# Performance work log

Measured on AMD Instinct MI355X. Metric: run time of the kernel, lower is better.

## Reference

```python
import jax, jax.numpy as jnp
import numpy as np


def _gumbel(key, shape):
    # -log(Exp(1)) == standard Gumbel; matches torch's -empty.exponential_().log()
    u = jax.random.uniform(key, shape, minval=1e-10, maxval=1.0)
    return -jnp.log(-jnp.log(u))


def setup_inputs() -> dict:
    key = jax.random.key(0)
    dims = [(1026, 1024), (3074, 1024), (5122, 512)]
    names = ['wc1', 'wc2', 'wd1', 'wd2', 'gc1', 'gc2', 'gd1', 'gd2']
    inp = {}
    k = key
    for li, (din, dout) in enumerate(dims, start=1):
        for nm in names:
            k, sub = jax.random.split(k)
            if nm.startswith('w'):
                inp[f'l{li}_{nm}'] = jax.random.normal(sub, (din, dout), dtype=jnp.float32)
            else:
                inp[f'l{li}_{nm}'] = _gumbel(sub, (din, dout)).astype(jnp.float32)
    k, kx, kw = jax.random.split(k, 3)
    inp['x'] = jax.random.uniform(kx, (32768, 512), dtype=jnp.float32)
    inp['lin_w'] = jax.random.uniform(kw, (1, 1024), dtype=jnp.float32)
    inp['tau'] = 1
    return inp


def _st_gate(w, g, tau):
    # hard gumbel-softmax over axis 0 with straight-through estimator
    y = jax.nn.softmax((w + g) / tau, axis=0)
    hard = jax.nn.one_hot(jnp.argmax(y, axis=0), w.shape[0], dtype=y.dtype).T
    return hard + y - jax.lax.stop_gradient(y)


def _logic_layer(h, ws, gs, tau, skip):
    wc1, wc2, wd1, wd2 = ws
    gc1, gc2, gd1, gd2 = gs
    c = (h @ _st_gate(wc1, gc1, tau)) * (h @ _st_gate(wc2, gc2, tau))  # AND
    a = h @ _st_gate(wd1, gd1, tau)
    b = h @ _st_gate(wd2, gd2, tau)
    d = 1.0 - (1.0 - a) * (1.0 - b)  # OR
    parts = [h, c, d] if skip else [c, d]
    return jnp.concatenate(parts, axis=-1)


def reference(x, l1_wc1, l1_wc2, l1_wd1, l1_wd2, l1_gc1, l1_gc2, l1_gd1, l1_gd2,
              l2_wc1, l2_wc2, l2_wd1, l2_wd2, l2_gc1, l2_gc2, l2_gd1, l2_gd2,
              l3_wc1, l3_wc2, l3_wd1, l3_wd2, l3_gc1, l3_gc2, l3_gd1, l3_gd2,
              lin_w, tau):
    t = jnp.asarray(tau, dtype=x.dtype)
    B = x.shape[0]
    # InputAugmentor: [x, 1-x, 1, 0]
    h = jnp.concatenate([x, 1.0 - x, jnp.ones((B, 1), x.dtype), jnp.zeros((B, 1), x.dtype)], axis=-1)
    layers = [
        ((l1_wc1, l1_wc2, l1_wd1, l1_wd2), (l1_gc1, l1_gc2, l1_gd1, l1_gd2), True),
        ((l2_wc1, l2_wc2, l2_wd1, l2_wd2), (l2_gc1, l2_gc2, l2_gd1, l2_gd2), True),
        ((l3_wc1, l3_wc2, l3_wd1, l3_wd2), (l3_gc1, l3_gc2, l3_gd1, l3_gd2), False),
    ]
    for ws, gs, skip in layers:
        h = _logic_layer(h, ws, gs, t, skip)
    # nonnegative == False -> weight used as-is
    return (h @ lin_w.T).squeeze(-1)
```

## Files before the change

kernel.cpp:

```cpp
#include <hip/hip_runtime.h>
#include <hip/hip_fp16.h>
#include <stdint.h>


struct GatePtrs {
    const float* w[12];
    const float* g[12];
};

__device__ __forceinline__ unsigned int sortkey(float f) {
    unsigned int u = __float_as_uint(f);
    return u ^ ((u & 0x80000000u) ? 0xFFFFFFFFu : 0x80000000u);
}

__global__ __launch_bounds__(256) void argmax_part(GatePtrs gp,
                                                   unsigned long long* __restrict__ part) {
    const int dins[3]  = {1026, 3074, 5122};
    const int douts[3] = {1024, 1024, 512};
    const int chs[3]   = {65, 193, 321};
    const int pbs[3]   = {0, 266240, 1056768};
    int gate = blockIdx.z, layer = gate >> 2, slot = gate & 3;
    int din = dins[layer], dout = douts[layer], ch = chs[layer];
    int s4    = dout >> 2;
    int cols4 = s4;
    int sub   = threadIdx.x / cols4;
    int c4    = threadIdx.x - sub * cols4;
    int chunk = blockIdx.y * (256 / cols4) + sub;
    if (chunk >= ch) return;
    int r0 = chunk * 16;
    int n  = min(16, din - r0);
    const float4* __restrict__ wp = (const float4*)gp.w[gate] + (size_t)r0 * s4 + c4;
    const float4* __restrict__ gq = (const float4*)gp.g[gate] + (size_t)r0 * s4 + c4;
    float bx = -3.4e38f, by = bx, bz = bx, bw = bx;
    int ix = r0, iy = r0, iz = r0, iw = r0;
    if (n == 16) {
        #pragma unroll
        for (int u = 0; u < 4; ++u) {
            float4 wv[4], gv[4];
            #pragma unroll
            for (int k = 0; k < 4; ++k) {
                wv[k] = wp[(size_t)(u * 4 + k) * s4];
                gv[k] = gq[(size_t)(u * 4 + k) * s4];
            }
            #pragma unroll
            for (int k = 0; k < 4; ++k) {
                int i = r0 + u * 4 + k;
                float vx = wv[k].x + gv[k].x, vy = wv[k].y + gv[k].y;
                float vz = wv[k].z + gv[k].z, vw = wv[k].w + gv[k].w;
                if (vx > bx) { bx = vx; ix = i; }
                if (vy > by) { by = vy; iy = i; }
                if (vz > bz) { bz = vz; iz = i; }
                if (vw > bw) { bw = vw; iw = i; }
            }
        }
    } else {
        for (int m = 0; m < n; ++m) {
            float4 wv = wp[(size_t)m * s4];
            float4 gv = gq[(size_t)m * s4];
            int i = r0 + m;
            float vx = wv.x + gv.x, vy = wv.y + gv.y;
            float vz = wv.z + gv.z, vw = wv.w + gv.w;
            if (vx > bx) { bx = vx; ix = i; }
            if (vy > by) { by = vy; iy = i; }
            if (vz > bz) { bz = vz; iz = i; }
            if (vw > bw) { bw = vw; iw = i; }
        }
    }
    unsigned long long* dst = part + pbs[layer]
                            + ((size_t)(slot * ch + chunk)) * dout + 4 * c4;
    dst[0] = ((unsigned long long)sortkey(bx) << 32) | (unsigned int)ix;
    dst[1] = ((unsigned long long)sortkey(by) << 32) | (unsigned int)iy;
    dst[2] = ((unsigned long long)sortkey(bz) << 32) | (unsigned int)iz;
    dst[3] = ((unsigned long long)sortkey(bw) << 32) | (unsigned int)iw;
}

__global__ __launch_bounds__(256) void reduce_pairs2(const unsigned long long* __restrict__ part,
                                                     unsigned short* __restrict__ pf) {
    __shared__ unsigned long long red[256];
    int t = threadIdx.x;
    int k = t >> 5, gi = t & 31;
    int C = blockIdx.x * 32;
    int l, s, g0, half, dout, ch, pb;
    if (C < 4096)      { l = 0; s = C >> 10;          g0 = C & 1023;          half = 1024; dout = 1024; ch = 65;  pb = 0; }
    else if (C < 8192) { l = 1; s = (C - 4096) >> 10; g0 = (C - 4096) & 1023; half = 1024; dout = 1024; ch = 193; pb = 266240; }
    else               { l = 2; s = (C - 8192) >> 9;  g0 = (C - 8192) & 511;  half = 512;  dout = 512;  ch = 321; pb = 1056768; }
    int g = g0 + gi;
    const unsigned long long* __restrict__ p = part + pb + (size_t)(s * ch) * dout + g;
    unsigned long long best = 0;
    for (int c = k; c < ch; c += 8) {
        unsigned long long v = p[(size_t)c * dout];
        if ((unsigned int)(v >> 32) > (unsigned int)(best >> 32)) best = v;
    }
    red[t] = best;
    __syncthreads();
    #pragma unroll
    for (int st = 4; st >= 1; st >>= 1) {
        if (k < st) {
            unsigned long long o = red[t + st * 32];
            if ((unsigned int)(o >> 32) > (unsigned int)(best >> 32)) best = o;
            red[t] = best;
        }
        __syncthreads();
    }
    if (k == 0) {
        int type = s >> 1, e = s & 1;
        int j = 2 * (l * 2048 + type * half + g) + e;
        pf[j] = (unsigned short)best;
    }
}

__global__ __launch_bounds__(256) void argmax_atomic(GatePtrs gp,
                                                     unsigned long long* __restrict__ packed) {
    const int dins[3]  = {1026, 3074, 5122};
    const int douts[3] = {1024, 1024, 512};
    const int offs[3]  = {0, 4096, 8192};
    int gate = blockIdx.z, layer = gate >> 2;
    int din = dins[layer], dout = douts[layer];
    int c2 = blockIdx.x * 256 + threadIdx.x;
    int r0 = blockIdx.y * 64;
    if (2 * c2 >= dout || r0 >= din) return;
    int r1 = min(r0 + 64, din);
    const float* __restrict__ w = gp.w[gate];
    const float* __restrict__ g = gp.g[gate];
    float bx = -3.4e38f, by = -3.4e38f;
    int rx = r0, ry = r0;
    #pragma unroll 8
    for (int i = r0; i < r1; ++i) {
        float2 wv = *(const float2*)(w + (size_t)i * dout + 2 * c2);
        float2 gv = *(const float2*)(g + (size_t)i * dout + 2 * c2);
        float vx = wv.x + gv.x, vy = wv.y + gv.y;
        if (vx > bx) { bx = vx; rx = i; }
        if (vy > by) { by = vy; ry = i; }
    }
    unsigned long long* dst = packed + offs[layer] + (gate & 3) * dout + 2 * c2;
    atomicMax(dst, ((unsigned long long)sortkey(bx) << 32)
                   | (unsigned long long)(0xFFFFFFFFu - (unsigned int)rx));
    atomicMax(dst + 1, ((unsigned long long)sortkey(by) << 32)
                   | (unsigned long long)(0xFFFFFFFFu - (unsigned int)ry));
}

__global__ __launch_bounds__(256) void convert_fb(const unsigned long long* __restrict__ packed,
                                                  ushort2* __restrict__ pf) {
    int i = blockIdx.x * 256 + threadIdx.x;
    if (i >= 5120) return;
    int l    = (i < 2048) ? 0 : ((i < 4096) ? 1 : 2);
    int half = (l == 2) ? 512 : 1024;
    int r    = i - l * 2048;
    int type = (r >= half) ? 1 : 0;
    int g    = r - type * half;
    int o1   = l * 4096 + 2 * type * half + g;
    int o2   = o1 + half;
    unsigned int i1 = 0xFFFFFFFFu - (unsigned int)(packed[o1] & 0xFFFFFFFFull);
    unsigned int i2 = 0xFFFFFFFFu - (unsigned int)(packed[o2] & 0xFFFFFFFFull);
    pf[i] = make_ushort2((unsigned short)i1, (unsigned short)i2);
}

__device__ __forceinline__ __half2 bc(unsigned int u) { return __builtin_bit_cast(__half2, u); }
__device__ __forceinline__ unsigned int cb(__half2 h) { return __builtin_bit_cast(unsigned int, h); }

__device__ __forceinline__ uint2 gat(const char* hb, unsigned int s) {
    return *(const uint2*)(hb + (s << 3));
}
__device__ __forceinline__ uint2 andg(uint2 a, uint2 b) {
    return make_uint2(cb(__hmul2(bc(a.x), bc(b.x))), cb(__hmul2(bc(a.y), bc(b.y))));
}
__device__ __forceinline__ uint2 org(uint2 a, uint2 b) {
    __half2 one = __float2half2_rn(1.0f);
    __half2 lo = __hsub2(one, __hmul2(__hsub2(one, bc(a.x)), __hsub2(one, bc(b.x))));
    __half2 hi = __hsub2(one, __hmul2(__hsub2(one, bc(a.y)), __hsub2(one, bc(b.y))));
    return make_uint2(cb(lo), cb(hi));
}

__global__ __launch_bounds__(512) void forward_kernel(const float* __restrict__ x,
                                                      const float* __restrict__ lin_w,
                                                      const ushort2* __restrict__ pairs,
                                                      float* __restrict__ out) {
    __shared__ uint2 h[5122];
    __shared__ float4 red[8];
    const int t  = threadIdx.x;
    const int r0 = blockIdx.x * 4;
    const char* hb = (const char*)h;

    float xa = x[(size_t)(r0 + 0) * 512 + t];
    float xb = x[(size_t)(r0 + 1) * 512 + t];
    float xc = x[(size_t)(r0 + 2) * 512 + t];
    float xd = x[(size_t)(r0 + 3) * 512 + t];
    ushort2 pa0 = pairs[t], pa1 = pairs[512 + t];
    ushort2 po0 = pairs[1024 + t], po1 = pairs[1536 + t];
    h[t]       = make_uint2(cb(__floats2half2_rn(xa, xb)), cb(__floats2half2_rn(xc, xd)));
    h[512 + t] = make_uint2(cb(__floats2half2_rn(1.f - xa, 1.f - xb)),
                            cb(__floats2half2_rn(1.f - xc, 1.f - xd)));
    if (t == 0) {
        unsigned int o = cb(__float2half2_rn(1.0f));
        h[1024] = make_uint2(o, o);
        h[1025] = make_uint2(0u, 0u);
    }
    __syncthreads();

    {
        uint2 a0 = andg(gat(hb, pa0.x), gat(hb, pa0.y));
        uint2 a1 = andg(gat(hb, pa1.x), gat(hb, pa1.y));
        uint2 o0 = org(gat(hb, po0.x), gat(hb, po0.y));
        uint2 o1 = org(gat(hb, po1.x), gat(hb, po1.y));
        h[1026 + t] = a0; h[1538 + t] = a1;
        h[2050 + t] = o0; h[2562 + t] = o1;
    }
    ushort2 qa0 = pairs[2048 + t], qa1 = pairs[2560 + t];
    ushort2 qo0 = pairs[3072 + t], qo1 = pairs[3584 + t];
    __syncthreads();

    {
        uint2 a0 = andg(gat(hb, qa0.x), gat(hb, qa0.y));
        uint2 a1 = andg(gat(hb, qa1.x), gat(hb, qa1.y));
        uint2 o0 = org(gat(hb, qo0.x), gat(hb, qo0.y));
        uint2 o1 = org(gat(hb, qo1.x), gat(hb, qo1.y));
        h[3074 + t] = a0; h[3586 + t] = a1;
        h[4098 + t] = o0; h[4610 + t] = o1;
    }
    ushort2 za = pairs[4096 + t], zo = pairs[4608 + t];
    float wA = lin_w[t], wO = lin_w[512 + t];
    __syncthreads();

    uint2 cg = andg(gat(hb, za.x), gat(hb, za.y));
    uint2 dg = org(gat(hb, zo.x), gat(hb, zo.y));
    float2 cl = __half22float2(bc(cg.x)), ch2 = __half22float2(bc(cg.y));
    float2 dl = __half22float2(bc(dg.x)), dh = __half22float2(bc(dg.y));
    float4 s;
    s.x = wA * cl.x  + wO * dl.x;
    s.y = wA * cl.y  + wO * dl.y;
    s.z = wA * ch2.x + wO * dh.x;
    s.w = wA * ch2.y + wO * dh.y;

    #pragma unroll
    for (int off = 32; off > 0; off >>= 1) {
        s.x += __shfl_down(s.x, off, 64);
        s.y += __shfl_down(s.y, off, 64);
        s.z += __shfl_down(s.z, off, 64);
        s.w += __shfl_down(s.w, off, 64);
    }
    if ((t & 63) == 0) red[t >> 6] = s;
    __syncthreads();
    if (t == 0) {
        float4 tot = red[0];
        #pragma unroll
        for (int i = 1; i < 8; ++i) {
            tot.x += red[i].x; tot.y += red[i].y;
            tot.z += red[i].z; tot.w += red[i].w;
        }
        *(float4*)(out + r0) = tot;
    }
}

extern "C" void kernel_launch(void* const* d_in, const int* in_sizes, int n_in,
                              void* d_out, int out_size, void* d_ws, size_t ws_size,
                              hipStream_t stream) {
    GatePtrs gp;
    for (int l = 0; l < 3; ++l)
        for (int s = 0; s < 4; ++s) {
            gp.w[l * 4 + s] = (const float*)d_in[l * 8 + s];
            gp.g[l * 4 + s] = (const float*)d_in[l * 8 + 4 + s];
        }
    const float* x     = (const float*)d_in[24];
    const float* lin_w = (const float*)d_in[25];
    float* out = (float*)d_out;

    const size_t partBytes = 1714176ull * 8ull;
    if (ws_size >= partBytes + 20480) {
        unsigned long long* part = (unsigned long long*)d_ws;
        unsigned short* pf = (unsigned short*)((char*)d_ws + partBytes);
        dim3 ga(1, 193, 12);
        argmax_part<<<ga, 256, 0, stream>>>(gp, part);
        reduce_pairs2<<<320, 256, 0, stream>>>(part, pf);
        forward_kernel<<<8192, 512, 0, stream>>>(x, lin_w, (const ushort2*)pf, out);
    } else {
        unsigned long long* packed = (unsigned long long*)d_ws;
        ushort2* pf = (ushort2*)((char*)d_ws + 10240 * 8);
        hipMemsetAsync(d_ws, 0, 10240 * 8, stream);
        dim3 ga(2, 81, 12);
        argmax_atomic<<<ga, 256, 0, stream>>>(gp, packed);
        convert_fb<<<20, 256, 0, stream>>>(packed, pf);
        forward_kernel<<<8192, 512, 0, stream>>>(x, lin_w, (const ushort2*)pf, out);
    }
}
```

Measured before the change: 342.8 us.

## Flatten argmax grid and split each 16-row chunk across sub-groups with LDS reduce

The argmax partial kernel moves from a 3D grid, which launched many idle blocks (193 y-blocks for every gate even when a layer has fewer chunks), to a flat 1D grid of exactly the needed blocks. Each block now holds 512 threads, and the 16 rows of a chunk are split across several thread sub-groups. Their partial results are then combined through shared memory. This removes wasted blocks and shortens each thread's serial load chain, at the cost of a __syncthreads and an LDS reduction step.

```diff
diff --git a/kernel.cpp b/kernel.cpp
--- a/kernel.cpp
+++ b/kernel.cpp
@@ -13,65 +13,69 @@
     return u ^ ((u & 0x80000000u) ? 0xFFFFFFFFu : 0x80000000u);
 }
 
-__global__ __launch_bounds__(256) void argmax_part(GatePtrs gp,
+__global__ __launch_bounds__(512) void argmax_part(GatePtrs gp,
                                                    unsigned long long* __restrict__ part) {
+    __shared__ unsigned long long red[1536];
     const int dins[3]  = {1026, 3074, 5122};
-    const int douts[3] = {1024, 1024, 512};
     const int chs[3]   = {65, 193, 321};
     const int pbs[3]   = {0, 266240, 1056768};
-    int gate = blockIdx.z, layer = gate >> 2, slot = gate & 3;
-    int din = dins[layer], dout = douts[layer], ch = chs[layer];
-    int s4    = dout >> 2;
-    int cols4 = s4;
-    int sub   = threadIdx.x / cols4;
-    int c4    = threadIdx.x - sub * cols4;
-    int chunk = blockIdx.y * (256 / cols4) + sub;
-    if (chunk >= ch) return;
-    int r0 = chunk * 16;
-    int n  = min(16, din - r0);
-    const float4* __restrict__ wp = (const float4*)gp.w[gate] + (size_t)r0 * s4 + c4;
-    const float4* __restrict__ gq = (const float4*)gp.g[gate] + (size_t)r0 * s4 + c4;
+    int bid = blockIdx.x, tid = threadIdx.x;
+    int layer, slot, chunk;
+    if (bid < 260)       { layer = 0; slot = bid / 65;  chunk = bid - slot * 65; }
+    else if (bid < 1032) { layer = 1; int r = bid - 260;  slot = r / 193; chunk = r - slot * 193; }
+    else                 { layer = 2; int r = bid - 1032; slot = r / 321; chunk = r - slot * 321; }
+    const int gate = layer * 4 + slot;
+    const int din = dins[layer], ch = chs[layer];
+    const int dout  = (layer == 2) ? 512 : 1024;
+    const int shift = (layer == 2) ? 7 : 8;
+    const int cols4 = 1 << shift;
+    const int subs  = 512 >> shift;
+    const int rps   = 16 / subs;
+    const int sub   = tid >> shift;
+    const int c4    = tid & (cols4 - 1);
+    const int s4    = dout >> 2;
+    const int r0    = chunk * 16;
+    const int rbeg  = r0 + sub * rps;
+    const int rend  = min(rbeg + rps, din);
+
+    const float4* __restrict__ wp = (const float4*)gp.w[gate] + (size_t)rbeg * s4 + c4;
+    const float4* __restrict__ gq = (const float4*)gp.g[gate] + (size_t)rbeg * s4 + c4;
     float bx = -3.4e38f, by = bx, bz = bx, bw = bx;
-    int ix = r0, iy = r0, iz = r0, iw = r0;
-    if (n == 16) {
-        #pragma unroll
-        for (int u = 0; u < 4; ++u) {
-            float4 wv[4], gv[4];
-            #pragma unroll
-            for (int k = 0; k < 4; ++k) {
-                wv[k] = wp[(size_t)(u * 4 + k) * s4];
-                gv[k] = gq[(size_t)(u * 4 + k) * s4];
-            }
-            #pragma unroll
-            for (int k = 0; k < 4; ++k) {
-                int i = r0 + u * 4 + k;
-                float vx = wv[k].x + gv[k].x, vy = wv[k].y + gv[k].y;
-                float vz = wv[k].z + gv[k].z, vw = wv[k].w + gv[k].w;
-                if (vx > bx) { bx = vx; ix = i; }
-                if (vy > by) { by = vy; iy = i; }
-                if (vz > bz) { bz = vz; iz = i; }
-                if (vw > bw) { bw = vw; iw = i; }
-            }
-        }
-    } else {
-        for (int m = 0; m < n; ++m) {
-            float4 wv = wp[(size_t)m * s4];
-            float4 gv = gq[(size_t)m * s4];
-            int i = r0 + m;
-            float vx = wv.x + gv.x, vy = wv.y + gv.y;
-            float vz = wv.z + gv.z, vw = wv.w + gv.w;
-            if (vx > bx) { bx = vx; ix = i; }
-            if (vy > by) { by = vy; iy = i; }
-            if (vz > bz) { bz = vz; iz = i; }
-            if (vw > bw) { bw = vw; iw = i; }
-        }
-    }
-    unsigned long long* dst = part + pbs[layer]
-                            + ((size_t)(slot * ch + chunk)) * dout + 4 * c4;
-    dst[0] = ((unsigned long long)sortkey(bx) << 32) | (unsigned int)ix;
-    dst[1] = ((unsigned long long)sortkey(by) << 32) | (unsigned int)iy;
-    dst[2] = ((unsigned long long)sortkey(bz) << 32) | (unsigned int)iz;
-    dst[3] = ((unsigned long long)sortkey(bw) << 32) | (unsigned int)iw;
+    int ix = rbeg, iy = rbeg, iz = rbeg, iw = rbeg;
+    #pragma unroll 4
+    for (int i = rbeg; i < rend; ++i) {
+        float4 wv = wp[(size_t)(i - rbeg) * s4];
+        float4 gv = gq[(size_t)(i - rbeg) * s4];
+        float vx = wv.x + gv.x, vy = wv.y + gv.y;
+        float vz = wv.z + gv.z, vw = wv.w + gv.w;
+        if (vx > bx) { bx = vx; ix = i; }
+        if (vy > by) { by = vy; iy = i; }
+        if (vz > bz) { bz = vz; iz = i; }
+        if (vw > bw) { bw = vw; iw = i; }
+    }
+    unsigned long long e0 = ((unsigned long long)sortkey(bx) << 32) | (unsigned int)ix;
+    unsigned long long e1 = ((unsigned long long)sortkey(by) << 32) | (unsigned int)iy;
+    unsigned long long e2 = ((unsigned long long)sortkey(bz) << 32) | (unsigned int)iz;
+    unsigned long long e3 = ((unsigned long long)sortkey(bw) << 32) | (unsigned int)iw;
+
+    if (sub != 0) {
+        unsigned long long* r = red + ((size_t)(sub - 1) * cols4 + c4) * 4;
+        r[0] = e0; r[1] = e1; r[2] = e2; r[3] = e3;
+    }
+    __syncthreads();
+    if (sub == 0) {
+        for (int s = 1; s < subs; ++s) {
+            const unsigned long long* r = red + ((size_t)(s - 1) * cols4 + c4) * 4;
+            unsigned long long o0 = r[0], o1 = r[1], o2 = r[2], o3 = r[3];
+            if ((unsigned int)(o0 >> 32) > (unsigned int)(e0 >> 32)) e0 = o0;
+            if ((unsigned int)(o1 >> 32) > (unsigned int)(e1 >> 32)) e1 = o1;
+            if ((unsigned int)(o2 >> 32) > (unsigned int)(e2 >> 32)) e2 = o2;
+            if ((unsigned int)(o3 >> 32) > (unsigned int)(e3 >> 32)) e3 = o3;
+        }
+        unsigned long long* dst = part + pbs[layer]
+                                + ((size_t)(slot * ch + chunk)) * dout + 4 * c4;
+        dst[0] = e0; dst[1] = e1; dst[2] = e2; dst[3] = e3;
+    }
 }
 
 __global__ __launch_bounds__(256) void reduce_pairs2(const unsigned long long* __restrict__ part,
@@ -268,8 +272,7 @@
     if (ws_size >= partBytes + 20480) {
         unsigned long long* part = (unsigned long long*)d_ws;
         unsigned short* pf = (unsigned short*)((char*)d_ws + partBytes);
-        dim3 ga(1, 193, 12);
-        argmax_part<<<ga, 256, 0, stream>>>(gp, part);
+        argmax_part<<<2316, 512, 0, stream>>>(gp, part);
         reduce_pairs2<<<320, 256, 0, stream>>>(part, pf);
         forward_kernel<<<8192, 512, 0, stream>>>(x, lin_w, (const ushort2*)pf, out);
     } else {
```

Measured after the change: 342.1 us. No clear change (-0.2%).
